# Optimization experiments

Measured on AMD Instinct MI355X. Metric: run time of the kernel, lower is better.

The kernel has to match this reference:

```python
import jax, jax.numpy as jnp
import numpy as np

B, S, QD, DM, H = 8, 4096, 4, 1024, 16
HD = DM // H
NROT = 4
EPS_LN = 1e-5


def layer_norm(x, g, b):
    m = x.mean(axis=-1, keepdims=True)
    v = ((x - m) ** 2).mean(axis=-1, keepdims=True)
    return (x - m) / jnp.sqrt(v + EPS_LN) * g + b


def quat_normalize(q):
    return q / (jnp.linalg.norm(q, axis=-1, keepdims=True) + 1e-8)


def quat_multiply(a, b):
    w1, x1, y1, z1 = a[..., 0], a[..., 1], a[..., 2], a[..., 3]
    w2, x2, y2, z2 = b[..., 0], b[..., 1], b[..., 2], b[..., 3]
    return jnp.stack([
        w1 * w2 - x1 * x2 - y1 * y2 - z1 * z2,
        w1 * x2 + x1 * w2 + y1 * z2 - z1 * y2,
        w1 * y2 - x1 * z2 + y1 * w2 + z1 * x2,
        w1 * z2 + x1 * y2 - y1 * x2 + z1 * w2,
    ], axis=-1)


def quat_conjugate(q):
    return q * jnp.array([1.0, -1.0, -1.0, -1.0], dtype=q.dtype)


def unit_quaternion(theta):  # theta: [3]
    c0, c1, c2 = jnp.cos(theta[0] / 2), jnp.cos(theta[1] / 2), jnp.cos(theta[2] / 2)
    s0, s1, s2 = jnp.sin(theta[0] / 2), jnp.sin(theta[1] / 2), jnp.sin(theta[2] / 2)
    q = jnp.stack([c0 * c1 * c2, s0 * c1 * c2, c0 * s1 * c2, c0 * c1 * s2])
    return quat_normalize(q)


def fractal_alpha(x):  # x: [B, S, DM] -> alpha: [B]
    xf = x.reshape(x.shape[0], -1)
    ps = jnp.abs(jnp.fft.rfft(xf, axis=-1)) ** 2  # [B, N/2+1]
    freqs = jnp.fft.rfftfreq(xf.shape[-1]).astype(x.dtype)
    w = ((freqs > 0.01) & (freqs < 0.5)).astype(x.dtype)
    n = w.sum()
    log_k = jnp.log(freqs + 1e-10)
    log_P = jnp.log(ps + 1e-10)
    mk = (w * log_k).sum() / n
    mP = (w * log_P).sum(axis=-1) / n  # [B]
    dk = (log_k - mk)
    cov = (w * dk * (log_P - mP[:, None])).sum(axis=-1)
    var = (w * dk * dk).sum()
    beta = -cov / (var + 1e-10)
    D = jnp.clip((3.0 - beta) / 2.0, 0.5, 1.5)
    # alpha(D) = alpha_base*(1 + lambda*(D - D_e)/D_e), base=1.0, lambda=0.8, D_e=1.0
    return jnp.clip(1.0 * (1.0 + 0.8 * (D - 1.0)), 0.1, 3.0)


def spectral_attention(x, alpha_base, phase_shift, W_attn_out, b_attn_out, ln_g, ln_b):
    # x: [B, S, DM]
    alpha = jax.lax.stop_gradient(fractal_alpha(x))  # [B]  (torch.no_grad)
    xh = x.reshape(B, S, H, HD).transpose(0, 2, 1, 3)  # [B, H, S, HD]
    x_fft = jnp.fft.fft(xh, axis=2)  # complex [B, H, S, HD]
    freqs = jnp.fft.fftfreq(S).astype(x.dtype)  # [S]
    log_k = jnp.log(jnp.abs(freqs) + 1e-8)
    log_kn = (log_k - log_k.mean()) / (jnp.std(log_k, ddof=1) + 1e-8)
    gelu_k = jax.nn.gelu(log_kn, approximate=False)  # [S]
    # phase[b,h,s] = alpha_base[h]*alpha[b]*gelu_k[s] + phase_shift[h]
    phase = (alpha_base[None, :, None] * alpha[:, None, None] * gelu_k[None, None, :]
             + phase_shift[None, :, None])  # [B, H, S]
    kernel = jnp.exp(1j * phase.astype(jnp.float32))[..., None]  # [B, H, S, 1]
    x_filt = jnp.fft.ifft(x_fft * kernel, axis=2).real  # [B, H, S, HD]
    out = x_filt.transpose(0, 2, 1, 3).reshape(B, S, DM)
    out = out @ W_attn_out + b_attn_out  # out_proj; dropout = identity (eval)
    return layer_norm(x + out, ln_g, ln_b)


def so4_evolution(q, theta_L, theta_R):  # q: [B, S, 4]
    out = q
    for i in range(NROT):
        qL = unit_quaternion(theta_L[i])
        qR_conj = quat_conjugate(unit_quaternion(theta_R[i]))
        out = quat_multiply(quat_multiply(jnp.broadcast_to(qL, out.shape), out),
                            jnp.broadcast_to(qR_conj, out.shape))
        out = quat_normalize(out)
    return out


def setup_inputs() -> dict:
    key = jax.random.key(0)
    ks = jax.random.split(key, 24)
    def rn(k, shape, scale=0.02):
        return jax.random.normal(k, shape, dtype=jnp.float32) * scale
    return {
        "x": jax.random.normal(ks[0], (B, S, QD), dtype=jnp.float32),
        "W_in": rn(ks[1], (QD, DM)), "b_in": jnp.zeros((DM,), jnp.float32),
        "alpha_base": jnp.ones((H,), jnp.float32),
        "phase_shift": jnp.zeros((H,), jnp.float32),
        "W_attn_out": rn(ks[2], (DM, DM)), "b_attn_out": jnp.zeros((DM,), jnp.float32),
        "ln_attn_g": jnp.ones((DM,), jnp.float32), "ln_attn_b": jnp.zeros((DM,), jnp.float32),
        "W_out": rn(ks[3], (DM, QD)), "b_out": jnp.zeros((QD,), jnp.float32),
        "theta_L": rn(ks[4], (NROT, 3), 0.1), "theta_R": rn(ks[5], (NROT, 3), 0.1),
        "W_ff1": rn(ks[6], (QD, 4 * QD)), "b_ff1": jnp.zeros((4 * QD,), jnp.float32),
        "W_ff2": rn(ks[7], (4 * QD, QD)), "b_ff2": jnp.zeros((QD,), jnp.float32),
        "n1_g": jnp.ones((QD,), jnp.float32), "n1_b": jnp.zeros((QD,), jnp.float32),
        "n2_g": jnp.ones((QD,), jnp.float32), "n2_b": jnp.zeros((QD,), jnp.float32),
        "n3_g": jnp.ones((QD,), jnp.float32), "n3_b": jnp.zeros((QD,), jnp.float32),
    }


def reference(x, W_in, b_in, alpha_base, phase_shift, W_attn_out, b_attn_out,
              ln_attn_g, ln_attn_b, W_out, b_out, theta_L, theta_R,
              W_ff1, b_ff1, W_ff2, b_ff2, n1_g, n1_b, n2_g, n2_b, n3_g, n3_b):
    x_proj = x @ W_in + b_in  # [B, S, DM]
    attn = spectral_attention(x_proj, alpha_base, phase_shift, W_attn_out, b_attn_out,
                              ln_attn_g, ln_attn_b)
    attn_quat = attn @ W_out + b_out  # [B, S, 4]
    h = quat_normalize(layer_norm(x + attn_quat, n1_g, n1_b))
    evolved = so4_evolution(h, theta_L, theta_R)
    h = quat_normalize(layer_norm(h + evolved, n2_g, n2_b))
    ff = jax.nn.gelu(h @ W_ff1 + b_ff1, approximate=False) @ W_ff2 + b_ff2
    h = quat_normalize(layer_norm(h + ff, n3_g, n3_b))
    return h
```

## Files before the change

kernel.cpp:

```cpp
#include <hip/hip_runtime.h>
#include <hip/hip_bf16.h>
#include <math.h>


#define DEV static __device__ __forceinline__
typedef unsigned int uint32;
typedef unsigned short u16;

typedef __attribute__((ext_vector_type(8))) _Float16 f16x8;
typedef __attribute__((ext_vector_type(4))) float f32x4;
typedef __attribute__((ext_vector_type(2))) unsigned int u32x2;

DEV float2 cmulf(float2 a, float2 b) {
  return make_float2(a.x * b.x - a.y * b.y, a.x * b.y + a.y * b.x);
}
DEV u16 f2h(float f) {
  union { _Float16 h; u16 u; } v;
  v.h = (_Float16)f;
  return v.u;
}
DEV float h2f(uint32 u) {
  union { u16 s; _Float16 h; } v;
  v.s = (u16)u;
  return (float)v.h;
}
DEV uint32 pack2h(float a, float b) {
  return (uint32)f2h(a) | ((uint32)f2h(b) << 16);
}
DEV float2 unp2h(uint32 u) {
  return make_float2(h2f(u & 0xFFFFu), h2f(u >> 16));
}
DEV void glds16(void* lds, const void* g) {
  __builtin_amdgcn_global_load_lds((const __attribute__((address_space(1))) unsigned int*)g,
                                   (__attribute__((address_space(3))) unsigned int*)lds, 16, 0, 0);
}
DEV void wave_sync() {
  asm volatile("s_waitcnt lgkmcnt(0)" ::: "memory");
  __builtin_amdgcn_sched_barrier(0);
}
DEV int dr10(int v) {
  int r = (int)(__brev((unsigned)v) >> 22);
  return ((r & 0x155) << 1) | ((r & 0x2AA) >> 1);
}
constexpr int dr6c(int v) {
  return ((v & 3) << 4) | (v & 12) | ((v >> 4) & 3);
}

constexpr float CQ[17] = {
  1.0f, 0.995184726672197f, 0.980785280403230f, 0.956940335732209f,
  0.923879532511287f, 0.881921264348355f, 0.831469612302545f, 0.773010453362737f,
  0.707106781186548f, 0.634393284163645f, 0.555570233019602f, 0.471396736825998f,
  0.382683432365090f, 0.290284677254462f, 0.195090322016128f, 0.098017140329561f, 0.0f };
constexpr float twc64(int j) {
  return (j & 63) <= 16 ? CQ[j & 63]
       : (j & 63) <= 32 ? -CQ[32 - (j & 63)]
       : (j & 63) <= 48 ? -CQ[(j & 63) - 32] : CQ[64 - (j & 63)];
}
constexpr float tws64(int j) {
  return (j & 63) <= 16 ? CQ[16 - (j & 63)]
       : (j & 63) <= 32 ? CQ[(j & 63) - 16]
       : (j & 63) <= 48 ? -CQ[48 - (j & 63)] : -CQ[(j & 63) - 48];
}

constexpr float CR_C[16] = {
  1.0f, 0.980785280403230f, 0.923879532511287f, 0.831469612302545f,
  0.707106781186548f, 0.555570233019602f, 0.382683432365090f, 0.195090322016128f,
  0.0f, -0.195090322016128f, -0.382683432365090f, -0.555570233019602f,
  -0.707106781186548f, -0.831469612302545f, -0.923879532511287f, -0.980785280403230f };
constexpr float CR_S[16] = {
  0.0f, 0.195090322016128f, 0.382683432365090f, 0.555570233019602f,
  0.707106781186548f, 0.831469612302545f, 0.923879532511287f, 0.980785280403230f,
  1.0f, 0.980785280403230f, 0.923879532511287f, 0.831469612302545f,
  0.707106781186548f, 0.555570233019602f, 0.382683432365090f, 0.195090322016128f };

template<int SGN>
DEV void rdif64(float2* z) {
  #pragma unroll
  for (int j = 0; j < 16; ++j) {
    float2 x0 = z[j], x1 = z[j + 16], x2 = z[j + 32], x3 = z[j + 48];
    float2 s0 = make_float2(x0.x + x2.x, x0.y + x2.y);
    float2 s1 = make_float2(x0.x - x2.x, x0.y - x2.y);
    float2 s2 = make_float2(x1.x + x3.x, x1.y + x3.y);
    float2 d  = make_float2(x1.x - x3.x, x1.y - x3.y);
    float2 s3 = (SGN < 0) ? make_float2(d.y, -d.x) : make_float2(-d.y, d.x);
    z[j] = make_float2(s0.x + s2.x, s0.y + s2.y);
    const float2 tf1 = make_float2(twc64(j),     (float)SGN * tws64(j));
    const float2 tf2 = make_float2(twc64(2 * j), (float)SGN * tws64(2 * j));
    const float2 tf3 = make_float2(twc64(3 * j), (float)SGN * tws64(3 * j));
    z[j + 16] = cmulf(make_float2(s1.x + s3.x, s1.y + s3.y), tf1);
    z[j + 32] = cmulf(make_float2(s0.x - s2.x, s0.y - s2.y), tf2);
    z[j + 48] = cmulf(make_float2(s1.x - s3.x, s1.y - s3.y), tf3);
  }
  #pragma unroll
  for (int b = 0; b < 64; b += 16)
    #pragma unroll
    for (int j = 0; j < 4; ++j) {
      const int i = b + j;
      float2 x0 = z[i], x1 = z[i + 4], x2 = z[i + 8], x3 = z[i + 12];
      float2 s0 = make_float2(x0.x + x2.x, x0.y + x2.y);
      float2 s1 = make_float2(x0.x - x2.x, x0.y - x2.y);
      float2 s2 = make_float2(x1.x + x3.x, x1.y + x3.y);
      float2 d  = make_float2(x1.x - x3.x, x1.y - x3.y);
      float2 s3 = (SGN < 0) ? make_float2(d.y, -d.x) : make_float2(-d.y, d.x);
      z[i] = make_float2(s0.x + s2.x, s0.y + s2.y);
      const float2 tf1 = make_float2(twc64(4 * j),  (float)SGN * tws64(4 * j));
      const float2 tf2 = make_float2(twc64(8 * j),  (float)SGN * tws64(8 * j));
      const float2 tf3 = make_float2(twc64(12 * j), (float)SGN * tws64(12 * j));
      z[i + 4]  = cmulf(make_float2(s1.x + s3.x, s1.y + s3.y), tf1);
      z[i + 8]  = cmulf(make_float2(s0.x - s2.x, s0.y - s2.y), tf2);
      z[i + 12] = cmulf(make_float2(s1.x - s3.x, s1.y - s3.y), tf3);
    }
  #pragma unroll
  for (int b = 0; b < 64; b += 4) {
    float2 x0 = z[b], x1 = z[b + 1], x2 = z[b + 2], x3 = z[b + 3];
    float2 s0 = make_float2(x0.x + x2.x, x0.y + x2.y);
    float2 s1 = make_float2(x0.x - x2.x, x0.y - x2.y);
    float2 s2 = make_float2(x1.x + x3.x, x1.y + x3.y);
    float2 d  = make_float2(x1.x - x3.x, x1.y - x3.y);
    float2 s3 = (SGN < 0) ? make_float2(d.y, -d.x) : make_float2(-d.y, d.x);
    z[b]     = make_float2(s0.x + s2.x, s0.y + s2.y);
    z[b + 1] = make_float2(s1.x + s3.x, s1.y + s3.y);
    z[b + 2] = make_float2(s0.x - s2.x, s0.y - s2.y);
    z[b + 3] = make_float2(s1.x - s3.x, s1.y - s3.y);
  }
}

template<int SGN>
DEV void rdit64(float2* z) {
  #pragma unroll
  for (int b = 0; b < 64; b += 4) {
    float2 b0 = z[b], b1 = z[b + 1], b2 = z[b + 2], b3 = z[b + 3];
    float2 t0 = make_float2(b0.x + b2.x, b0.y + b2.y);
    float2 t1 = make_float2(b0.x - b2.x, b0.y - b2.y);
    float2 t2 = make_float2(b1.x + b3.x, b1.y + b3.y);
    float2 d  = make_float2(b1.x - b3.x, b1.y - b3.y);
    float2 t3 = (SGN > 0) ? make_float2(-d.y, d.x) : make_float2(d.y, -d.x);
    z[b]     = make_float2(t0.x + t2.x, t0.y + t2.y);
    z[b + 1] = make_float2(t1.x + t3.x, t1.y + t3.y);
    z[b + 2] = make_float2(t0.x - t2.x, t0.y - t2.y);
    z[b + 3] = make_float2(t1.x - t3.x, t1.y - t3.y);
  }
  #pragma unroll
  for (int b = 0; b < 64; b += 16)
    #pragma unroll
    for (int j = 0; j < 4; ++j) {
      const int i = b + j;
      const float2 tf1 = make_float2(twc64(4 * j),  (float)SGN * tws64(4 * j));
      const float2 tf2 = make_float2(twc64(8 * j),  (float)SGN * tws64(8 * j));
      const float2 tf3 = make_float2(twc64(12 * j), (float)SGN * tws64(12 * j));
      float2 b0 = z[i];
      float2 b1 = cmulf(z[i + 4], tf1);
      float2 b2 = cmulf(z[i + 8], tf2);
      float2 b3 = cmulf(z[i + 12], tf3);
      float2 t0 = make_float2(b0.x + b2.x, b0.y + b2.y);
      float2 t1 = make_float2(b0.x - b2.x, b0.y - b2.y);
      float2 t2 = make_float2(b1.x + b3.x, b1.y + b3.y);
      float2 d  = make_float2(b1.x - b3.x, b1.y - b3.y);
      float2 t3 = (SGN > 0) ? make_float2(-d.y, d.x) : make_float2(d.y, -d.x);
      z[i]      = make_float2(t0.x + t2.x, t0.y + t2.y);
      z[i + 4]  = make_float2(t1.x + t3.x, t1.y + t3.y);
      z[i + 8]  = make_float2(t0.x - t2.x, t0.y - t2.y);
      z[i + 12] = make_float2(t1.x - t3.x, t1.y - t3.y);
    }
  #pragma unroll
  for (int j = 0; j < 16; ++j) {
    const float2 tf1 = make_float2(twc64(j),     (float)SGN * tws64(j));
    const float2 tf2 = make_float2(twc64(2 * j), (float)SGN * tws64(2 * j));
    const float2 tf3 = make_float2(twc64(3 * j), (float)SGN * tws64(3 * j));
    float2 b0 = z[j];
    float2 b1 = cmulf(z[j + 16], tf1);
    float2 b2 = cmulf(z[j + 32], tf2);
    float2 b3 = cmulf(z[j + 48], tf3);
    float2 t0 = make_float2(b0.x + b2.x, b0.y + b2.y);
    float2 t1 = make_float2(b0.x - b2.x, b0.y - b2.y);
    float2 t2 = make_float2(b1.x + b3.x, b1.y + b3.y);
    float2 d  = make_float2(b1.x - b3.x, b1.y - b3.y);
    float2 t3 = (SGN > 0) ? make_float2(-d.y, d.x) : make_float2(d.y, -d.x);
    z[j]      = make_float2(t0.x + t2.x, t0.y + t2.y);
    z[j + 16] = make_float2(t1.x + t3.x, t1.y + t3.y);
    z[j + 32] = make_float2(t0.x - t2.x, t0.y - t2.y);
    z[j + 48] = make_float2(t1.x - t3.x, t1.y - t3.y);
  }
}

template<int L, int NLOG, int NSUB, bool WL>
DEV void dif4_stages(float2* F, int lg) {
  #pragma unroll
  for (int st = 0; st < NLOG / 2; ++st) {
    const int qlog = NLOG - 2 - 2 * st;
    const int q = 1 << qlog;
    float bs, bc;
    __sincosf((float)(lg & (q - 1)) * (-1.57079632679489661923f / (float)q), &bs, &bc);
    const float2 base = make_float2(bc, bs);
    #pragma unroll
    for (int u = 0; u < NSUB * (1 << (NLOG - 2)) / L; ++u) {
      const int sub = (u * L) >> (NLOG - 2);
      const int bf = ((u * L) & ((1 << (NLOG - 2)) - 1)) + lg;
      const int jj = ((u * L) % q) * 8 / q;
      const int i1 = (sub << NLOG) + ((bf >> qlog) << (qlog + 2)) + (bf & (q - 1));
      float2 x0 = F[i1], x1 = F[i1 + q], x2 = F[i1 + 2 * q], x3 = F[i1 + 3 * q];
      float2 s0 = make_float2(x0.x + x2.x, x0.y + x2.y);
      float2 s1 = make_float2(x0.x - x2.x, x0.y - x2.y);
      float2 s2 = make_float2(x1.x + x3.x, x1.y + x3.y);
      float2 dq = make_float2(x1.x - x3.x, x1.y - x3.y);
      float2 s3 = make_float2(dq.y, -dq.x);
      F[i1] = make_float2(s0.x + s2.x, s0.y + s2.y);
      if (qlog == 0) {
        F[i1 + 1] = make_float2(s1.x + s3.x, s1.y + s3.y);
        F[i1 + 2] = make_float2(s0.x - s2.x, s0.y - s2.y);
        F[i1 + 3] = make_float2(s1.x - s3.x, s1.y - s3.y);
      } else {
        const float2 tf1 = (jj == 0) ? base : cmulf(base, make_float2(CR_C[jj], -CR_S[jj]));
        const float2 tf2 = cmulf(tf1, tf1);
        const float2 tf3 = cmulf(tf2, tf1);
        F[i1 + q]     = cmulf(make_float2(s1.x + s3.x, s1.y + s3.y), tf1);
        F[i1 + 2 * q] = cmulf(make_float2(s0.x - s2.x, s0.y - s2.y), tf2);
        F[i1 + 3 * q] = cmulf(make_float2(s1.x - s3.x, s1.y - s3.y), tf3);
      }
    }
    if (WL) wave_sync(); else __syncthreads();
  }
}

DEV float4 qmul4(float4 a, float4 b) {
  return make_float4(
    a.x * b.x - a.y * b.y - a.z * b.z - a.w * b.w,
    a.x * b.y + a.y * b.x + a.z * b.w - a.w * b.z,
    a.x * b.z - a.y * b.w + a.z * b.x + a.w * b.y,
    a.x * b.w + a.y * b.z - a.z * b.y + a.w * b.x);
}
DEV float4 qne(float4 q) {
  float n = sqrtf(q.x * q.x + q.y * q.y + q.z * q.z + q.w * q.w) + 1e-8f;
  float r = 1.0f / n;
  return make_float4(q.x * r, q.y * r, q.z * r, q.w * r);
}

__global__ __launch_bounds__(512) void kx_fr_pass1(const float* __restrict__ x,
    const float* __restrict__ W_in, const float* __restrict__ b_in,
    uint32* __restrict__ zmid) {
  __shared__ float2 fb[8 * 1028];
  const int t = threadIdx.x, l = t & 63, w = t >> 6;
  const int btile = blockIdx.x, bz = blockIdx.y;
  const int bcol = btile * 8 + w;
  const int d = 2 * (bcol & 511);
  const int soff = bcol >> 9;
  const float w00 = W_in[d],     w10 = W_in[1024 + d], w20 = W_in[2048 + d], w30 = W_in[3072 + d];
  const float w01 = W_in[d + 1], w11 = W_in[1025 + d], w21 = W_in[2049 + d], w31 = W_in[3073 + d];
  const float bi0 = b_in[d], bi1 = b_in[d + 1];
  const float* xb = x + (size_t)bz * 4096 * 4;
  float2* fbw = fb + w * 1028;
  #pragma unroll
  for (int i = 0; i < 16; ++i) {
    int a = i * 64 + l;
    int s = 4 * a + soff;
    float4 xv = *(const float4*)(xb + (size_t)s * 4);
    float z0 = fmaf(xv.x, w00, fmaf(xv.y, w10, fmaf(xv.z, w20, fmaf(xv.w, w30, bi0))));
    float z1 = fmaf(xv.x, w01, fmaf(xv.y, w11, fmaf(xv.z, w21, fmaf(xv.w, w31, bi1))));
    fbw[a] = make_float2(z0, z1);
  }
  wave_sync();
  dif4_stages<64, 10, 1, true>(fbw, l);
  __syncthreads();
  uint32* dst = zmid + (size_t)bz * (1024 * 2048);
  #pragma unroll
  for (int i = 0; i < 16; ++i) {
    int idx = i * 512 + t;
    int w8 = idx & 7, cnat = idx >> 3;
    float2 v = fb[w8 * 1028 + dr10(cnat)];
    dst[(size_t)cnat * 2048 + btile * 8 + w8] = pack2h(v.x, v.y);
  }
}

DEV float block_reduce128(float* red, int t, float v) {
  red[t] = v; __syncthreads();
  for (int s = 64; s; s >>= 1) { if (t < s) red[t] += red[t + s]; __syncthreads(); }
  float r = red[0]; __syncthreads();
  return r;
}

__global__ __launch_bounds__(128) void kx_fr_pass2(const uint32* __restrict__ zmid,
    float* __restrict__ partials, float* __restrict__ sparts) {
  __shared__ float2 fb[2 * 2048];
  const int t = threadIdx.x, l = t & 63, w = t >> 6;
  const int cg = blockIdx.x, bz = blockIdx.y;
  const int c = (cg == 0) ? (w ? 512 : 0) : (w ? (1024 - cg) : cg);
  const uint32* src = zmid + ((size_t)bz * 1024 + c) * 2048;
  float2* fbc = fb + w * 2048;
  float2 rot[4], stp4;
  {
    float sn, cs;
    __sincosf((float)(l * c) * (-6.28318530717958647692f / 2097152.0f), &sn, &cs);
    rot[0] = make_float2(cs, sn);
    float2 stp;
    __sincosf((float)c * (-6.28318530717958647692f / 32768.0f), &sn, &cs);
    stp = make_float2(cs, sn);
    rot[1] = cmulf(rot[0], stp);
    float2 stp2 = cmulf(stp, stp);
    rot[2] = cmulf(rot[0], stp2);
    rot[3] = cmulf(rot[1], stp2);
    stp4 = cmulf(stp2, stp2);
  }
  float2 zr[32];
  #pragma unroll
  for (int i = 0; i < 32; ++i) {
    int bb = i * 64 + l;
    zr[i] = cmulf(unp2h(src[bb]), rot[i & 3]);
    rot[i & 3] = cmulf(rot[i & 3], stp4);
  }
  {
    float bs, bc;
    __sincosf((float)l * (-3.14159265358979323846f / 1024.0f), &bs, &bc);
    const float2 b2 = make_float2(bc, bs);
    #pragma unroll
    for (int u = 0; u < 16; ++u) {
      const float2 tf = (u == 0) ? b2 : cmulf(b2, make_float2(CR_C[u], -CR_S[u]));
      int i1 = u * 64 + l;
      float2 a0 = zr[u], a1 = zr[u + 16];
      fbc[i1] = make_float2(a0.x + a1.x, a0.y + a1.y);
      fbc[i1 + 1024] = cmulf(make_float2(a0.x - a1.x, a0.y - a1.y), tf);
    }
    wave_sync();
  }
  dif4_stages<64, 10, 2, true>(fbc, l);
  __syncthreads();
  float t0 = 0.f, t1 = 0.f, s0 = 0.f, s1 = 0.f, s2 = 0.f;
  if (cg != 0) {
    const float2* fbm = fb + (1 - w) * 2048;
    float2 pw[32];
    pw[0] = make_float2(1.f, 0.f);
    {
      float sn, cs;
      __sincosf(-3.14159265358979323846f / 2048.0f, &sn, &cs);
      float2 w1 = make_float2(cs, sn);
      #pragma unroll
      for (int j = 1; j < 32; ++j) pw[j] = cmulf(pw[j - 1], w1);
    }
    const int drl = (l & 3) * 256 + ((l >> 2) & 3) * 64 + ((l >> 4) & 3) * 16;
    float2 base2;
    {
      float sn, cs;
      __sincosf((float)drl * (-3.14159265358979323846f / 1024.0f), &sn, &cs);
      float2 lf = make_float2(cs, sn);
      __sincosf((float)c * (-6.28318530717958647692f / 4194304.0f), &sn, &cs);
      base2 = cmulf(make_float2(cs, sn), lf);
    }
    #pragma unroll
    for (int i = 0; i < 32; ++i) {
      const int p = i * 64 + l;
      const int dri = (i & 3) * 4 + ((i >> 2) & 3);
      const int top = i >> 4;
      const int dd = 2 * (drl + dri) + top;
      float2 Zk = fbc[p];
      float2 Zm = fbm[2047 - p];
      float2 E = make_float2(0.5f * (Zk.x + Zm.x), 0.5f * (Zk.y - Zm.y));
      float2 A = make_float2(Zk.x - Zm.x, Zk.y + Zm.y);
      float2 O = make_float2(0.5f * A.y, -0.5f * A.x);
      float2 urot = cmulf(base2, pw[2 * dri + top]);
      float2 U = cmulf(urot, O);
      float Xr = E.x + U.x, Xi = E.y + U.y;
      float P = Xr * Xr + Xi * Xi;
      int k = c + (dd << 10);
      float fr = (float)k * (1.0f / 4194304.0f);
      if (fr > 0.01f && fr < 0.5f) {
        float lp = __logf(P + 1e-10f);
        float lk = __logf(fr + 1e-10f);
        t0 += lp; t1 += lk * lp;
        s0 += 1.0f; s1 += lk; s2 += lk * lk;
      }
    }
  } else {
    const float2* fbm = fbc;
    float2 urot;
    {
      float sn, cs;
      __sincosf((float)(c + l * 1024) * (-6.28318530717958647692f / 4194304.0f), &sn, &cs);
      urot = make_float2(cs, sn);
    }
    const float2 ustp = make_float2(0.995184726672197f, -0.0980171403295606f);
    #pragma unroll
    for (int i = 0; i < 32; ++i) {
      int dd = i * 64 + l;
      int md = (c == 0) ? ((2048 - dd) & 2047) : (2047 - dd);
      int pk = ((dd & 1) << 10) | dr10(dd >> 1);
      int pm = ((md & 1) << 10) | dr10(md >> 1);
      float2 Zk = fbc[pk];
      float2 Zm = fbm[pm];
      float2 E = make_float2(0.5f * (Zk.x + Zm.x), 0.5f * (Zk.y - Zm.y));
      float2 A = make_float2(Zk.x - Zm.x, Zk.y + Zm.y);
      float2 O = make_float2(0.5f * A.y, -0.5f * A.x);
      float2 U = cmulf(urot, O);
      float Xr = E.x + U.x, Xi = E.y + U.y;
      float P = Xr * Xr + Xi * Xi;
      int k = c + (dd << 10);
      float fr = (float)k * (1.0f / 4194304.0f);
      if (fr > 0.01f && fr < 0.5f) {
        float lp = __logf(P + 1e-10f);
        float lk = __logf(fr + 1e-10f);
        t0 += lp; t1 += lk * lp;
        s0 += 1.0f; s1 += lk; s2 += lk * lk;
      }
      urot = cmulf(urot, ustp);
    }
  }
  __syncthreads();
  float* red = (float*)fb;
  float T0 = block_reduce128(red, t, t0);
  float T1 = block_reduce128(red, t, t1);
  if (t == 0) {
    partials[((size_t)bz * 512 + cg) * 2 + 0] = T0;
    partials[((size_t)bz * 512 + cg) * 2 + 1] = T1;
  }
  if (bz == 0) {
    float S0 = block_reduce128(red, t, s0);
    float S1 = block_reduce128(red, t, s1);
    float S2 = block_reduce128(red, t, s2);
    if (t == 0) { sparts[cg * 3] = S0; sparts[cg * 3 + 1] = S1; sparts[cg * 3 + 2] = S2; }
  }
}

DEV float block_reduce256s(float* sh, int t, float v) {
  sh[t] = v; __syncthreads();
  for (int s = 128; s; s >>= 1) { if (t < s) sh[t] += sh[t + s]; __syncthreads(); }
  float r = sh[0]; __syncthreads();
  return r;
}

__global__ __launch_bounds__(256) void kx_gainsall(const float* __restrict__ partials,
    const float* __restrict__ sparts, const float* __restrict__ abase,
    const float* __restrict__ pshift, const float* __restrict__ thL,
    const float* __restrict__ thR, const float* __restrict__ W,
    u16* __restrict__ Wt, float* __restrict__ gains, float* __restrict__ qlr) {
  const int bid = blockIdx.x;
  const int t = threadIdx.x;
  if (bid >= 128) {
    __shared__ float tile[64][65];
    const int q = bid - 128;
    const int nt = q & 15, dt = q >> 4;
    #pragma unroll
    for (int i = 0; i < 16; ++i) {
      int idx = i * 256 + t;
      int r = idx >> 6, cc = idx & 63;
      tile[r][cc] = W[(size_t)(dt * 64 + r) * 1024 + nt * 64 + cc];
    }
    __syncthreads();
    #pragma unroll
    for (int i = 0; i < 2; ++i) {
      int task = i * 256 + t;
      int nl = task >> 3, g = task & 7;
      union { u16 h[8]; uint4 v; } pk;
      #pragma unroll
      for (int k = 0; k < 8; ++k) pk.h[k] = f2h(tile[g * 8 + k][nl]);
      size_t idx = (size_t)(nt * 64 + nl) * 1024 + dt * 64 + ((g ^ (nl & 7)) << 3);
      *(uint4*)(Wt + idx) = pk.v;
    }
    return;
  }
  __shared__ float red[256];
  float s0 = 0.f, s1 = 0.f, s2 = 0.f;
  for (int i = t; i < 512; i += 256) {
    s0 += sparts[i * 3]; s1 += sparts[i * 3 + 1]; s2 += sparts[i * 3 + 2];
  }
  s0 = block_reduce256s(red, t, s0);
  s1 = block_reduce256s(red, t, s1);
  s2 = block_reduce256s(red, t, s2);
  const float mk = s1 / s0;
  const float var = s2 - mk * s1;
  const int b = bid >> 4, h = bid & 15;
  float t0 = 0.f, t1 = 0.f;
  for (int i = t; i < 512; i += 256) {
    t0 += partials[((size_t)b * 512 + i) * 2];
    t1 += partials[((size_t)b * 512 + i) * 2 + 1];
  }
  t0 = block_reduce256s(red, t, t0);
  t1 = block_reduce256s(red, t, t1);
  const float cov = t1 - mk * t0;
  const float beta = -cov / (var + 1e-10f);
  const float D = fminf(fmaxf((3.0f - beta) * 0.5f, 0.5f), 1.5f);
  const float alpha = fminf(fmaxf(1.0f + 0.8f * (D - 1.0f), 0.1f), 3.0f);
  const float aa = abase[h] * alpha;
  const float ps = pshift[h];
  float lkv[16];
  float ls = 0.f;
  #pragma unroll
  for (int i = 0; i < 16; ++i) {
    int s = i * 256 + t;
    int m = (s < 2048) ? s : (4096 - s);
    lkv[i] = logf((float)m * (1.0f / 4096.0f) + 1e-8f);
    ls += lkv[i];
  }
  const float mean = block_reduce256s(red, t, ls) * (1.0f / 4096.0f);
  float vs = 0.f;
  #pragma unroll
  for (int i = 0; i < 16; ++i) { float dv = lkv[i] - mean; vs += dv * dv; }
  const float sd = sqrtf(block_reduce256s(red, t, vs) * (1.0f / 4095.0f));
  for (int k = t; k < 2049; k += 256) {
    float lk_k = logf((float)k * (1.0f / 4096.0f) + 1e-8f);
    float xn = (lk_k - mean) / (sd + 1e-8f);
    float ge = 0.5f * xn * (1.0f + erff(xn * 0.70710678118654752440f));
    gains[(size_t)bid * 2064 + k] = cosf(fmaf(aa, ge, ps));
  }
  if (bid == 0 && t == 0) {
    float4 QL = make_float4(1.f, 0.f, 0.f, 0.f);
    float4 QRC = make_float4(1.f, 0.f, 0.f, 0.f);
    for (int it = 0; it < 4; ++it) {
      float ss0, cc0, ss1, cc1, ss2, cc2;
      sincosf(0.5f * thL[it * 3 + 0], &ss0, &cc0);
      sincosf(0.5f * thL[it * 3 + 1], &ss1, &cc1);
      sincosf(0.5f * thL[it * 3 + 2], &ss2, &cc2);
      float4 qL = qne(make_float4(cc0 * cc1 * cc2, ss0 * cc1 * cc2, cc0 * ss1 * cc2, cc0 * cc1 * ss2));
      QL = qmul4(qL, QL);
      sincosf(0.5f * thR[it * 3 + 0], &ss0, &cc0);
      sincosf(0.5f * thR[it * 3 + 1], &ss1, &cc1);
      sincosf(0.5f * thR[it * 3 + 2], &ss2, &cc2);
      float4 qR = qne(make_float4(cc0 * cc1 * cc2, ss0 * cc1 * cc2, cc0 * ss1 * cc2, cc0 * cc1 * ss2));
      QRC = qmul4(QRC, make_float4(qR.x, -qR.y, -qR.z, -qR.w));
    }
    *(float4*)qlr = QL;
    *(float4*)(qlr + 4) = QRC;
  }
}

__global__ __launch_bounds__(128, 1) void kx_filter(const float* __restrict__ x,
    const float* __restrict__ W_in, const float* __restrict__ b_in,
    const float* __restrict__ gains, uint32* __restrict__ XFp) {
  __shared__ uint32 tr[2][4096];
  const int t = threadIdx.x, l = t & 63, wv = t >> 6;
  const int g = blockIdx.x, h = blockIdx.y, bz = blockIdx.z;
  const int d0 = h * 64 + g * 4 + wv * 2;
  const float* gn = gains + ((size_t)bz * 16 + h) * 2064;
  const float wa0 = W_in[d0],     wa1 = W_in[1024 + d0], wa2 = W_in[2048 + d0], wa3 = W_in[3072 + d0];
  const float wb0 = W_in[d0 + 1], wb1 = W_in[1025 + d0], wb2 = W_in[2049 + d0], wb3 = W_in[3073 + d0];
  const float bia = b_in[d0], bib = b_in[d0 + 1];
  const float* xb = x + (size_t)bz * 4096 * 4;
  uint32* trw = tr[wv];
  float2 z[64];
  #pragma unroll
  for (int r = 0; r < 64; ++r) {
    int s = r * 64 + l;
    float4 xv = *(const float4*)(xb + (size_t)s * 4);
    float za = fmaf(xv.x, wa0, fmaf(xv.y, wa1, fmaf(xv.z, wa2, fmaf(xv.w, wa3, bia))));
    float zb = fmaf(xv.x, wb0, fmaf(xv.y, wb1, fmaf(xv.z, wb2, fmaf(xv.w, wb3, bib))));
    z[r] = make_float2(za, zb);
  }
  rdif64<-1>(z);
  {
    float sn, cs;
    __sincosf((float)l * (-6.28318530717958647692f / 4096.0f), &sn, &cs);
    float2 w1 = make_float2(cs, sn);
    float2 w2 = cmulf(w1, w1);
    float2 w4 = cmulf(w2, w2);
    float2 tch[4] = { make_float2(1.f, 0.f), w1, w2, cmulf(w2, w1) };
    #pragma unroll
    for (int i = 0; i < 16; ++i) {
      #pragma unroll
      for (int j = 0; j < 4; ++j) {
        const int rr = dr6c(4 * i + j);
        z[rr] = cmulf(z[rr], tch[j]);
      }
      #pragma unroll
      for (int j = 0; j < 4; ++j) tch[j] = cmulf(tch[j], w4);
    }
  }
  #pragma unroll
  for (int r = 0; r < 64; ++r) {
    const int k1 = dr6c(r);
    trw[k1 * 64 + ((l + k1) & 63)] = pack2h(z[r].x, z[r].y);
  }
  wave_sync();
  #pragma unroll
  for (int c = 0; c < 64; ++c) {
    uint32 u = trw[l * 64 + ((c + l) & 63)];
    z[c] = unp2h(u);
  }
  wave_sync();
  rdif64<-1>(z);
  #pragma unroll
  for (int r = 0; r < 64; ++r) {
    const int k = l + (dr6c(r) << 6);
    const int km = (k < 2048) ? k : (4096 - k);
    const float gk = gn[km];
    z[r] = make_float2(z[r].x * gk, z[r].y * gk);
  }
  rdit64<1>(z);
  {
    float sn, cs;
    __sincosf((float)l * (6.28318530717958647692f / 4096.0f), &sn, &cs);
    float2 v1 = make_float2(cs, sn);
    float2 v2 = cmulf(v1, v1);
    float2 v4 = cmulf(v2, v2);
    float2 tch[4] = { make_float2(1.f, 0.f), v1, v2, cmulf(v2, v1) };
    #pragma unroll
    for (int i = 0; i < 16; ++i) {
      #pragma unroll
      for (int j = 0; j < 4; ++j)
        z[4 * i + j] = cmulf(z[4 * i + j], tch[j]);
      #pragma unroll
      for (int j = 0; j < 4; ++j) tch[j] = cmulf(tch[j], v4);
    }
  }
  #pragma unroll
  for (int r = 0; r < 64; ++r)
    trw[r * 64 + ((l + r) & 63)] = pack2h(z[r].x, z[r].y);
  wave_sync();
  #pragma unroll
  for (int c = 0; c < 64; ++c) {
    uint32 u = trw[l * 64 + ((c + l) & 63)];
    z[c] = unp2h(u);
  }
  wave_sync();
  #pragma unroll
  for (int j = 0; j < 64; ++j) {
    const int dj = dr6c(j);
    if (dj > j) { float2 tmp = z[j]; z[j] = z[dj]; z[dj] = tmp; }
  }
  rdit64<1>(z);
  uint32* rowp = XFp + ((size_t)bz * 512 + (d0 >> 1)) * 4096;
  const float sc = 1.0f / 4096.0f;
  #pragma unroll
  for (int r = 0; r < 64; ++r)
    rowp[r * 64 + l] = pack2h(z[r].x * sc, z[r].y * sc);
}

__global__ __launch_bounds__(256) void kx_a16(const uint32* __restrict__ XFp, uint32* __restrict__ Aswz) {
  __shared__ uint32 tl[64][65];
  const int t = threadIdx.x;
  const int st = blockIdx.x, pt = blockIdx.y, bz = blockIdx.z;
  const uint32* src = XFp + ((size_t)bz * 512 + pt * 64) * 4096 + st * 64;
  #pragma unroll
  for (int i = 0; i < 16; ++i) {
    int p = i * 4 + (t >> 6);
    int s = t & 63;
    tl[p][s] = src[(size_t)p * 4096 + s];
  }
  __syncthreads();
  uint32* dst = Aswz + ((size_t)bz * 4096 + st * 64) * 512 + pt * 64;
  #pragma unroll
  for (int i = 0; i < 16; ++i) {
    int s = i * 4 + (t >> 6);
    int c = t & 63;
    int gsl = ((c & 31) >> 2) ^ (s & 7);
    int u32idx = (c >> 5) * 32 + gsl * 4 + (c & 3);
    dst[(size_t)s * 512 + u32idx] = tl[c][s];
  }
}

__global__ __launch_bounds__(256) void kx_gemm(const u16* __restrict__ A,
    const u16* __restrict__ Bw, u16* __restrict__ C) {
  __shared__ u16 sm[32768];
  const int t = threadIdx.x, l = t & 63, w = t >> 6;
  const int wm = w >> 1, wn = w & 1;
  const int id = blockIdx.x;
  const int wg = (id & 7) * 256 + (id >> 3);
  const int bm = wg >> 3, bn = wg & 7;
  const int bh = bm >> 5;
  const u16* Ab = A + ((size_t)(bh * 4096 + (bm & 31) * 128)) * 1024;
  const u16* Bb = Bw + (size_t)(bn * 128) * 1024;
  const int fr = l & 15;
  const int lr = l >> 3, lg = l & 7;
  f32x4 acc[4][4];
  #pragma unroll
  for (int m = 0; m < 4; ++m)
    #pragma unroll
    for (int n = 0; n < 4; ++n) acc[m][n] = (f32x4){0.f, 0.f, 0.f, 0.f};

  #define STAGE(KT, BUF) { \
    u16* Ad = sm + (BUF) * 8192; \
    u16* Bd = sm + 16384 + (BUF) * 8192; \
    _Pragma("unroll") \
    for (int j = 0; j < 4; ++j) { \
      int qq = j * 4 + w; \
      glds16((void*)(Ad + qq * 512), Ab + (size_t)(qq * 8 + lr) * 1024 + (KT) * 64 + lg * 8); \
      glds16((void*)(Bd + qq * 512), Bb + (size_t)(qq * 8 + lr) * 1024 + (KT) * 64 + lg * 8); \
    } }

  STAGE(0, 0);
  __syncthreads();
  for (int kt = 0; kt < 16; ++kt) {
    const int cur = kt & 1;
    if (kt < 15) STAGE(kt + 1, cur ^ 1);
    const u16* Ac = sm + cur * 8192;
    const u16* Bc = sm + 16384 + cur * 8192;
    #pragma unroll
    for (int kk = 0; kk < 2; ++kk) {
      const int g8r = kk * 4 + (l >> 4);
      f16x8 af[4], bf[4];
      #pragma unroll
      for (int m = 0; m < 4; ++m) {
        int s = wm * 64 + m * 16 + fr;
        af[m] = *(const f16x8*)&Ac[s * 64 + ((g8r ^ (s & 7)) << 3)];
      }
      #pragma unroll
      for (int n = 0; n < 4; ++n) {
        int nn = wn * 64 + n * 16 + fr;
        bf[n] = *(const f16x8*)&Bc[nn * 64 + ((g8r ^ (nn & 7)) << 3)];
      }
      #pragma unroll
      for (int m = 0; m < 4; ++m)
        #pragma unroll
        for (int n = 0; n < 4; ++n)
          acc[m][n] = __builtin_amdgcn_mfma_f32_16x16x32_f16(af[m], bf[n], acc[m][n], 0, 0, 0);
    }
    __syncthreads();
  }
  float* Cs = (float*)sm;
  const int rl4 = (l >> 4) * 4;
  #pragma unroll
  for (int m = 0; m < 4; ++m) {
    int rbase = wm * 64 + m * 16 + rl4;
    #pragma unroll
    for (int n = 0; n < 4; ++n) {
      int cc = wn * 64 + n * 16 + fr;
      #pragma unroll
      for (int e = 0; e < 4; ++e) {
        int r = rbase + e;
        Cs[r * 128 + (cc ^ (((r >> 2) & 3) << 3))] = acc[m][n][e];
      }
    }
  }
  __syncthreads();
  u16* cgp = C + (size_t)(bm * 128) * 1024 + bn * 128;
  #pragma unroll
  for (int it = 0; it < 16; ++it) {
    int idx = it * 256 + t;
    int r = idx >> 5, c4 = (idx & 31) * 4;
    f32x4 v = *(const f32x4*)&Cs[r * 128 + (c4 ^ (((r >> 2) & 3) << 3))];
    u32x2 pv;
    pv.x = (uint32)f2h(v.x) | ((uint32)f2h(v.y) << 16);
    pv.y = (uint32)f2h(v.z) | ((uint32)f2h(v.w) << 16);
    __builtin_nontemporal_store(pv, (u32x2*)(cgp + (size_t)r * 1024 + c4));
  }
}

DEV float wred64(float v) {
  #pragma unroll
  for (int m = 32; m; m >>= 1) v += __shfl_xor(v, m);
  return v;
}
DEV float4 ln4q(float4 v, const float* g, const float* b) {
  float m = 0.25f * (v.x + v.y + v.z + v.w);
  float a0 = v.x - m, a1 = v.y - m, a2 = v.z - m, a3 = v.w - m;
  float var = 0.25f * (a0 * a0 + a1 * a1 + a2 * a2 + a3 * a3);
  float rs = 1.0f / sqrtf(var + 1e-5f);
  return make_float4(a0 * rs * g[0] + b[0], a1 * rs * g[1] + b[1],
                     a2 * rs * g[2] + b[2], a3 * rs * g[3] + b[3]);
}
DEV float gelu1(float v) { return 0.5f * v * (1.0f + erff(v * 0.70710678118654752440f)); }

__global__ __launch_bounds__(256) void kx_tail(const u16* __restrict__ G,
    const float* __restrict__ x, const float* __restrict__ W_in, const float* __restrict__ b_in,
    const float* __restrict__ b_attn, const float* __restrict__ lng, const float* __restrict__ lnb,
    const float* __restrict__ W_out, const float* __restrict__ b_out,
    const float* __restrict__ qlr,
    const float* __restrict__ Wf1, const float* __restrict__ bff1,
    const float* __restrict__ Wf2, const float* __restrict__ bff2,
    const float* __restrict__ n1g, const float* __restrict__ n1b,
    const float* __restrict__ n2g, const float* __restrict__ n2b,
    const float* __restrict__ n3g, const float* __restrict__ n3b,
    float* __restrict__ out) {
  const int l = threadIdx.x & 63, w = threadIdx.x >> 6;
  const size_t rg = (size_t)blockIdx.x * 4 + w;
  const float4 x4 = *(const float4*)(x + rg * 4);
  float4 tv[4];
  float lsum = 0.f;
  #pragma unroll
  for (int j = 0; j < 4; ++j) {
    int dd = j * 256 + l * 4;
    uint2 gv = *(const uint2*)(G + rg * 1024 + dd);
    float4 g4 = make_float4(h2f(gv.x & 0xFFFFu), h2f(gv.x >> 16),
                            h2f(gv.y & 0xFFFFu), h2f(gv.y >> 16));
    float4 w0 = *(const float4*)(W_in + dd);
    float4 w1 = *(const float4*)(W_in + 1024 + dd);
    float4 w2 = *(const float4*)(W_in + 2048 + dd);
    float4 w3 = *(const float4*)(W_in + 3072 + dd);
    float4 bi = *(const float4*)(b_in + dd);
    float4 ba = *(const float4*)(b_attn + dd);
    float4 o;
    o.x = g4.x + bi.x + ba.x + x4.x * w0.x + x4.y * w1.x + x4.z * w2.x + x4.w * w3.x;
    o.y = g4.y + bi.y + ba.y + x4.x * w0.y + x4.y * w1.y + x4.z * w2.y + x4.w * w3.y;
    o.z = g4.z + bi.z + ba.z + x4.x * w0.z + x4.y * w1.z + x4.z * w2.z + x4.w * w3.z;
    o.w = g4.w + bi.w + ba.w + x4.x * w0.w + x4.y * w1.w + x4.z * w2.w + x4.w * w3.w;
    tv[j] = o;
    lsum += o.x + o.y + o.z + o.w;
  }
  const float mean = wred64(lsum) * (1.0f / 1024.0f);
  float vsum = 0.f;
  #pragma unroll
  for (int j = 0; j < 4; ++j) {
    float a0 = tv[j].x - mean, a1 = tv[j].y - mean, a2 = tv[j].z - mean, a3 = tv[j].w - mean;
    vsum += a0 * a0 + a1 * a1 + a2 * a2 + a3 * a3;
  }
  const float rstd = 1.0f / sqrtf(wred64(vsum) * (1.0f / 1024.0f) + 1e-5f);
  float4 aq = make_float4(0.f, 0.f, 0.f, 0.f);
  #pragma unroll
  for (int j = 0; j < 4; ++j) {
    int dd = j * 256 + l * 4;
    float4 gg = *(const float4*)(lng + dd);
    float4 bb = *(const float4*)(lnb + dd);
    float av[4];
    av[0] = (tv[j].x - mean) * rstd * gg.x + bb.x;
    av[1] = (tv[j].y - mean) * rstd * gg.y + bb.y;
    av[2] = (tv[j].z - mean) * rstd * gg.z + bb.z;
    av[3] = (tv[j].w - mean) * rstd * gg.w + bb.w;
    #pragma unroll
    for (int e = 0; e < 4; ++e) {
      float4 wr = *(const float4*)(W_out + (size_t)(dd + e) * 4);
      aq.x = fmaf(av[e], wr.x, aq.x);
      aq.y = fmaf(av[e], wr.y, aq.y);
      aq.z = fmaf(av[e], wr.z, aq.z);
      aq.w = fmaf(av[e], wr.w, aq.w);
    }
  }
  aq.x = wred64(aq.x) + b_out[0];
  aq.y = wred64(aq.y) + b_out[1];
  aq.z = wred64(aq.z) + b_out[2];
  aq.w = wred64(aq.w) + b_out[3];
  float4 q1 = make_float4(x4.x + aq.x, x4.y + aq.y, x4.z + aq.z, x4.w + aq.w);
  float4 hq = qne(ln4q(q1, n1g, n1b));
  const float4 QL = *(const float4*)qlr;
  const float4 QRC = *(const float4*)(qlr + 4);
  float4 o = qne(qmul4(qmul4(QL, hq), QRC));
  float4 h2 = qne(ln4q(make_float4(hq.x + o.x, hq.y + o.y, hq.z + o.z, hq.w + o.w), n2g, n2b));
  float ffx = 0.f, ffy = 0.f, ffz = 0.f, ffw = 0.f;
  if (l < 16) {
    float uv = bff1[l] + h2.x * Wf1[l] + h2.y * Wf1[16 + l] + h2.z * Wf1[32 + l] + h2.w * Wf1[48 + l];
    uv = gelu1(uv);
    float4 w2r = *(const float4*)(Wf2 + l * 4);
    ffx = uv * w2r.x; ffy = uv * w2r.y; ffz = uv * w2r.z; ffw = uv * w2r.w;
  }
  ffx = wred64(ffx) + bff2[0];
  ffy = wred64(ffy) + bff2[1];
  ffz = wred64(ffz) + bff2[2];
  ffw = wred64(ffw) + bff2[3];
  float4 h3 = qne(ln4q(make_float4(h2.x + ffx, h2.y + ffy, h2.z + ffz, h2.w + ffw), n3g, n3b));
  if (l == 0) *(float4*)(out + rg * 4) = h3;
}

extern "C" void kernel_launch(void* const* d_in, const int* in_sizes, int n_in,
                              void* d_out, int out_size, void* d_ws, size_t ws_size,
                              hipStream_t stream) {
  (void)in_sizes; (void)n_in; (void)out_size;
  const float* x      = (const float*)d_in[0];
  const float* W_in   = (const float*)d_in[1];
  const float* b_in   = (const float*)d_in[2];
  const float* abase  = (const float*)d_in[3];
  const float* pshift = (const float*)d_in[4];
  const float* Wattn  = (const float*)d_in[5];
  const float* battn  = (const float*)d_in[6];
  const float* lng    = (const float*)d_in[7];
  const float* lnb    = (const float*)d_in[8];
  const float* Wout   = (const float*)d_in[9];
  const float* bout   = (const float*)d_in[10];
  const float* thL    = (const float*)d_in[11];
  const float* thR    = (const float*)d_in[12];
  const float* Wf1    = (const float*)d_in[13];
  const float* bff1   = (const float*)d_in[14];
  const float* Wf2    = (const float*)d_in[15];
  const float* bff2   = (const float*)d_in[16];
  const float* n1g    = (const float*)d_in[17];
  const float* n1b    = (const float*)d_in[18];
  const float* n2g    = (const float*)d_in[19];
  const float* n2b    = (const float*)d_in[20];
  const float* n3g    = (const float*)d_in[21];
  const float* n3b    = (const float*)d_in[22];

  if (ws_size < (size_t)138459204) return;
  char* ws = (char*)d_ws;
  uint32* Zmid  = (uint32*)ws;
  uint32* XFp   = (uint32*)ws;
  u16*   Aswz   = (u16*)(ws + 67108864);
  u16*   C16    = (u16*)ws;
  u16*   W2h    = (u16*)(ws + 134217728);
  float* gainsw = (float*)(ws + 136314880);
  float* qlrw   = (float*)(ws + 137400320);
  float* partials = (float*)(ws + 138412032);
  float* sparts   = (float*)(ws + 138444800);

  kx_fr_pass1<<<dim3(256, 8), 512, 0, stream>>>(x, W_in, b_in, Zmid);
  kx_fr_pass2<<<dim3(512, 8), 128, 0, stream>>>(Zmid, partials, sparts);
  kx_gainsall<<<384, 256, 0, stream>>>(partials, sparts, abase, pshift, thL, thR,
                                       Wattn, W2h, gainsw, qlrw);
  kx_filter<<<dim3(16, 16, 8), 128, 0, stream>>>(x, W_in, b_in, gainsw, XFp);
  kx_a16<<<dim3(64, 8, 8), 256, 0, stream>>>(XFp, (uint32*)Aswz);
  kx_gemm<<<2048, 256, 0, stream>>>(Aswz, W2h, C16);
  kx_tail<<<8192, 256, 0, stream>>>(C16, x, W_in, b_in, battn, lng, lnb, Wout, bout,
                                    qlrw, Wf1, bff1, Wf2, bff2,
                                    n1g, n1b, n2g, n2b, n3g, n3b, (float*)d_out);
}
```

Baseline: 417.9 us.

## Fuse transpose kernel into GEMM by loading transposed A tiles directly

Removes the separate kx_a16 transpose/swizzle kernel. The GEMM now reads the filter output XFp in its native [pair, s] layout into LDS with an XOR swizzle, and builds each A fragment from four 32-bit LDS reads across k-pairs. This drops a 64 MB round trip through global memory and one kernel launch. In exchange, A-fragment LDS reads become four scalar loads instead of one 128-bit load, which adds LDS instruction pressure inside the MFMA loop.

Result: faster. 395.2 us (-5.4%).

```diff
diff --git a/kernel.cpp b/kernel.cpp
--- a/kernel.cpp
+++ b/kernel.cpp
@@ -29,6 +29,11 @@
 }
 DEV float2 unp2h(uint32 u) {
   return make_float2(h2f(u & 0xFFFFu), h2f(u >> 16));
+}
+DEV f16x8 mkfrag4(uint32 a, uint32 b, uint32 c, uint32 d) {
+  union { uint4 u; f16x8 v; } x;
+  x.u = make_uint4(a, b, c, d);
+  return x.v;
 }
 DEV void glds16(void* lds, const void* g) {
   __builtin_amdgcn_global_load_lds((const __attribute__((address_space(1))) unsigned int*)g,
@@ -621,42 +626,24 @@
     rowp[r * 64 + l] = pack2h(z[r].x * sc, z[r].y * sc);
 }
 
-__global__ __launch_bounds__(256) void kx_a16(const uint32* __restrict__ XFp, uint32* __restrict__ Aswz) {
-  __shared__ uint32 tl[64][65];
-  const int t = threadIdx.x;
-  const int st = blockIdx.x, pt = blockIdx.y, bz = blockIdx.z;
-  const uint32* src = XFp + ((size_t)bz * 512 + pt * 64) * 4096 + st * 64;
-  #pragma unroll
-  for (int i = 0; i < 16; ++i) {
-    int p = i * 4 + (t >> 6);
-    int s = t & 63;
-    tl[p][s] = src[(size_t)p * 4096 + s];
-  }
-  __syncthreads();
-  uint32* dst = Aswz + ((size_t)bz * 4096 + st * 64) * 512 + pt * 64;
-  #pragma unroll
-  for (int i = 0; i < 16; ++i) {
-    int s = i * 4 + (t >> 6);
-    int c = t & 63;
-    int gsl = ((c & 31) >> 2) ^ (s & 7);
-    int u32idx = (c >> 5) * 32 + gsl * 4 + (c & 3);
-    dst[(size_t)s * 512 + u32idx] = tl[c][s];
-  }
-}
-
-__global__ __launch_bounds__(256) void kx_gemm(const u16* __restrict__ A,
+__global__ __launch_bounds__(256) void kx_gemm(const uint32* __restrict__ XFp,
     const u16* __restrict__ Bw, u16* __restrict__ C) {
-  __shared__ u16 sm[32768];
+  __shared__ uint32 sm[16384];
+  uint32* Asm = sm;
+  u16* Bsm = (u16*)(sm + 8192);
   const int t = threadIdx.x, l = t & 63, w = t >> 6;
   const int wm = w >> 1, wn = w & 1;
   const int id = blockIdx.x;
   const int wg = (id & 7) * 256 + (id >> 3);
   const int bm = wg >> 3, bn = wg & 7;
   const int bh = bm >> 5;
-  const u16* Ab = A + ((size_t)(bh * 4096 + (bm & 31) * 128)) * 1024;
+  const int s0 = (bm & 31) * 128;
+  const uint32* Ab = XFp + ((size_t)(bh * 512)) * 4096 + s0;
   const u16* Bb = Bw + (size_t)(bn * 128) * 1024;
   const int fr = l & 15;
   const int lr = l >> 3, lg = l & 7;
+  const int ap = (l >> 5);
+  const int ag = l & 31;
   f32x4 acc[4][4];
   #pragma unroll
   for (int m = 0; m < 4; ++m)
@@ -664,13 +651,16 @@
     for (int n = 0; n < 4; ++n) acc[m][n] = (f32x4){0.f, 0.f, 0.f, 0.f};
 
   #define STAGE(KT, BUF) { \
-    u16* Ad = sm + (BUF) * 8192; \
-    u16* Bd = sm + 16384 + (BUF) * 8192; \
+    uint32* Ad = Asm + (BUF) * 4096; \
+    u16* Bd = Bsm + (BUF) * 8192; \
     _Pragma("unroll") \
     for (int j = 0; j < 4; ++j) { \
-      int qq = j * 4 + w; \
-      glds16((void*)(Ad + qq * 512), Ab + (size_t)(qq * 8 + lr) * 1024 + (KT) * 64 + lg * 8); \
-      glds16((void*)(Bd + qq * 512), Bb + (size_t)(qq * 8 + lr) * 1024 + (KT) * 64 + lg * 8); \
+      int cch = j * 4 + w; \
+      int pp = 2 * cch + ap; \
+      int gs = ag ^ (pp & 7); \
+      glds16((void*)(Ad + cch * 256), Ab + (size_t)((KT) * 32 + pp) * 4096 + gs * 4); \
+      int q = j * 4 + w; \
+      glds16((void*)(Bd + q * 512), Bb + (size_t)(q * 8 + lr) * 1024 + (KT) * 64 + lg * 8); \
     } }
 
   STAGE(0, 0);
@@ -678,16 +668,22 @@
   for (int kt = 0; kt < 16; ++kt) {
     const int cur = kt & 1;
     if (kt < 15) STAGE(kt + 1, cur ^ 1);
-    const u16* Ac = sm + cur * 8192;
-    const u16* Bc = sm + 16384 + cur * 8192;
+    const uint32* Ac = Asm + cur * 4096;
+    const u16* Bc = Bsm + cur * 8192;
     #pragma unroll
     for (int kk = 0; kk < 2; ++kk) {
       const int g8r = kk * 4 + (l >> 4);
+      const int p0 = kk * 16 + (l >> 4) * 4;
       f16x8 af[4], bf[4];
       #pragma unroll
       for (int m = 0; m < 4; ++m) {
-        int s = wm * 64 + m * 16 + fr;
-        af[m] = *(const f16x8*)&Ac[s * 64 + ((g8r ^ (s & 7)) << 3)];
+        const int s = wm * 64 + m * 16 + fr;
+        const int sg = s >> 2, sr = s & 3;
+        uint32 q0 = Ac[(p0 + 0) * 128 + (((sg) ^ ((p0 + 0) & 7)) << 2) + sr];
+        uint32 q1 = Ac[(p0 + 1) * 128 + (((sg) ^ ((p0 + 1) & 7)) << 2) + sr];
+        uint32 q2 = Ac[(p0 + 2) * 128 + (((sg) ^ ((p0 + 2) & 7)) << 2) + sr];
+        uint32 q3 = Ac[(p0 + 3) * 128 + (((sg) ^ ((p0 + 3) & 7)) << 2) + sr];
+        af[m] = mkfrag4(q0, q1, q2, q3);
       }
       #pragma unroll
       for (int n = 0; n < 4; ++n) {
@@ -867,8 +863,7 @@
   char* ws = (char*)d_ws;
   uint32* Zmid  = (uint32*)ws;
   uint32* XFp   = (uint32*)ws;
-  u16*   Aswz   = (u16*)(ws + 67108864);
-  u16*   C16    = (u16*)ws;
+  u16*   C16    = (u16*)(ws + 67108864);
   u16*   W2h    = (u16*)(ws + 134217728);
   float* gainsw = (float*)(ws + 136314880);
   float* qlrw   = (float*)(ws + 137400320);
@@ -880,8 +875,7 @@
   kx_gainsall<<<384, 256, 0, stream>>>(partials, sparts, abase, pshift, thL, thR,
                                        Wattn, W2h, gainsw, qlrw);
   kx_filter<<<dim3(16, 16, 8), 128, 0, stream>>>(x, W_in, b_in, gainsw, XFp);
-  kx_a16<<<dim3(64, 8, 8), 256, 0, stream>>>(XFp, (uint32*)Aswz);
-  kx_gemm<<<2048, 256, 0, stream>>>(Aswz, W2h, C16);
+  kx_gemm<<<2048, 256, 0, stream>>>(XFp, W2h, C16);
   kx_tail<<<8192, 256, 0, stream>>>(C16, x, W_in, b_in, battn, lng, lnb, Wout, bout,
                                     qlrw, Wf1, bff1, Wf2, bff2,
                                     n1g, n1b, n2g, n2b, n3g, n3b, (float*)d_out);
```
